# Kernel optimization log

Hardware: AMD Instinct MI355X
Metric: run time of the kernel (lower is better)

The kernel has to match this reference:

```python
import jax, jax.numpy as jnp
import numpy as np

DIM = 512
HEADS = 8
HEAD_DIM = DIM // HEADS
SCALE = HEAD_DIM ** -0.5
EPS = 1e-5


def _layernorm(x, w, b):
    mu = jnp.mean(x, axis=-1, keepdims=True)
    var = jnp.mean(jnp.square(x - mu), axis=-1, keepdims=True)
    return (x - mu) * jax.lax.rsqrt(var + EPS) * w + b


def setup_inputs() -> dict:
    key = jax.random.key(0)
    ks = jax.random.split(key, 9)
    B, Hs, Ws = 8, 32, 32
    r = jax.random.normal(ks[0], (B, DIM, Hs, Ws), dtype=jnp.float32)
    z = jax.random.normal(ks[1], (B, DIM, Hs, Ws), dtype=jnp.float32)
    w = lambda k: jax.random.normal(k, (DIM, DIM), dtype=jnp.float32) * 0.02
    return {
        "r": r,
        "z": z,
        "norm_r_w": jnp.ones((DIM,), jnp.float32),
        "norm_r_b": jnp.zeros((DIM,), jnp.float32),
        "norm_z_w": jnp.ones((DIM,), jnp.float32),
        "norm_z_b": jnp.zeros((DIM,), jnp.float32),
        "Wq": w(ks[2]),  # [out, in] torch Linear convention, no bias (qkv_bias=False)
        "Wk": w(ks[3]),
        "Wv": w(ks[4]),
        "Wa": w(ks[5]),
        "Wproj": w(ks[6]),
        "bproj": jax.random.normal(ks[7], (DIM,), dtype=jnp.float32) * 0.02,
    }


def reference(r, z, norm_r_w, norm_r_b, norm_z_w, norm_z_b, Wq, Wk, Wv, Wa, Wproj, bproj):
    z_sc = z
    B, C, Hz, Wz = z.shape
    # flatten(2).permute(0,2,1): NCHW -> [B, N, C]
    rf = r.reshape(B, C, -1).transpose(0, 2, 1)  # [B, Nr, C]
    zf = z.reshape(B, C, -1).transpose(0, 2, 1)  # [B, Nz, C]
    Nr, Nz = rf.shape[1], zf.shape[1]

    rf = _layernorm(rf, norm_r_w, norm_r_b)
    zf = _layernorm(zf, norm_z_w, norm_z_b)

    def heads(x, W, N):  # torch Linear: x @ W.T, then split heads -> [B,H,N,D]
        return (x @ W.T).reshape(B, N, HEADS, HEAD_DIM).transpose(0, 2, 1, 3)

    q = heads(rf, Wq, Nr)  # [B,H,Nr,D]
    k = heads(rf, Wk, Nr)  # [B,H,Nr,D]
    v = heads(zf, Wv, Nz)  # [B,H,Nz,D]
    a = heads(zf, Wa, Nz)  # [B,H,Nz,D]

    # stage 1: softmax(k @ a^T) @ v  -> anchor-aggregated values per r-token
    attn1 = jax.nn.softmax(jnp.einsum('bhnd,bhmd->bhnm', k, a) * SCALE, axis=-1)  # [B,H,Nr,Nz]
    v1 = jnp.einsum('bhnm,bhmd->bhnd', attn1, v)  # [B,H,Nr,D]

    # stage 2: softmax(a @ q^T) @ v1 -> outputs aligned with z tokens
    attn2 = jax.nn.softmax(jnp.einsum('bhmd,bhnd->bhmn', a, q) * SCALE, axis=-1)  # [B,H,Nz,Nr]
    out = jnp.einsum('bhmn,bhnd->bhmd', attn2, v1)  # [B,H,Nz,D]

    out = out.transpose(0, 2, 1, 3).reshape(B, Nz, C)
    out = out @ Wproj.T + bproj
    out = out.transpose(0, 2, 1).reshape(B, C, Hz, Wz)
    return out + z_sc
```

## Files before the change

### kernel.cpp

```cpp
#include <hip/hip_runtime.h>
#include <hip/hip_bf16.h>
#include <stdint.h>


using bf16 = __bf16;
typedef __bf16 bf16x4 __attribute__((ext_vector_type(4)));
typedef __bf16 bf16x8 __attribute__((ext_vector_type(8)));
typedef float f32x4 __attribute__((ext_vector_type(4)));
typedef float f32x16 __attribute__((ext_vector_type(16)));

#define DIMC 512
#define NTOK 1024
#define NB 8
#define NH 8
#define HD 64
#define SLABS 16

__device__ __forceinline__ void gload_lds16(const bf16* g, bf16* l) {
  __builtin_amdgcn_global_load_lds((__attribute__((address_space(1))) void*)g,
                                   (__attribute__((address_space(3))) void*)l,
                                   16, 0, 0);
}

__device__ __forceinline__ float bpermf(int srclane, float v) {
  int i = __builtin_amdgcn_ds_bpermute(srclane << 2, __builtin_bit_cast(int, v));
  return __builtin_bit_cast(float, i);
}

__device__ __forceinline__ int pkbf(float lo, float hi) {
  unsigned short a = __builtin_bit_cast(unsigned short, (bf16)lo);
  unsigned short b = __builtin_bit_cast(unsigned short, (bf16)hi);
  return (int)((unsigned)a | ((unsigned)b << 16));
}

__device__ __forceinline__ float fexp2(float x) {
  float r;
  asm("v_exp_f32 %0, %1" : "=v"(r) : "v"(x));
  return r;
}

__global__ __launch_bounds__(256) void k_ln_part(
    const float* __restrict__ r, const float* __restrict__ z, float* __restrict__ part) {
  int slab = blockIdx.x, b = blockIdx.y, tensor = blockIdx.z;
  const float* x = (tensor ? z : r) + ((size_t)b * DIMC + slab * 32) * NTOK + threadIdx.x * 4;
  float4 s = {0, 0, 0, 0}, ss = {0, 0, 0, 0};
#pragma unroll 8
  for (int c = 0; c < 32; ++c) {
    float4 v = *reinterpret_cast<const float4*>(x + (size_t)c * NTOK);
    s.x += v.x; s.y += v.y; s.z += v.z; s.w += v.w;
    ss.x += v.x * v.x; ss.y += v.y * v.y; ss.z += v.z * v.z; ss.w += v.w * v.w;
  }
  float* p = part + (((size_t)(tensor * 8 + b) * SLABS + slab) * 2) * NTOK + threadIdx.x * 4;
  *reinterpret_cast<float4*>(p) = s;
  *reinterpret_cast<float4*>(p + NTOK) = ss;
}

__global__ __launch_bounds__(256) void k_ln_fin(
    const float* __restrict__ part, float* __restrict__ mu, float* __restrict__ rs) {
  int t = blockIdx.x * 256 + threadIdx.x;
  int tb = t >> 10, n = t & 1023;
  const float* p = part + (size_t)tb * SLABS * 2 * NTOK + n;
  float s = 0.f, ss = 0.f;
#pragma unroll
  for (int i = 0; i < SLABS; ++i) {
    s += p[(size_t)i * 2 * NTOK];
    ss += p[(size_t)i * 2 * NTOK + NTOK];
  }
  float m = s * (1.0f / DIMC);
  mu[t] = m;
  rs[t] = rsqrtf(ss * (1.0f / DIMC) - m * m + 1e-5f);
}

__global__ __launch_bounds__(256) void k_ln_apply(
    const float* __restrict__ r, const float* __restrict__ z,
    const float* __restrict__ wr, const float* __restrict__ br,
    const float* __restrict__ wz, const float* __restrict__ bz,
    const float* __restrict__ mu, const float* __restrict__ rs,
    bf16* __restrict__ rf, bf16* __restrict__ zf) {
  __shared__ __align__(16) bf16 T[64 * 72];
  int bt = blockIdx.z;
  int tensor = bt & 1, b = bt >> 1;
  const float* x   = tensor ? z  : r;
  const float* w   = tensor ? wz : wr;
  const float* bia = tensor ? bz : br;
  bf16* out = tensor ? zf : rf;
  int n0 = blockIdx.x * 64, c0 = blockIdx.y * 64;
  const float* muP = mu + (tensor << 13) + (b << 10) + n0;
  const float* rsP = rs + (tensor << 13) + (b << 10) + n0;
  int tid = threadIdx.x;
  int cl = tid >> 3;
  int nl = (tid & 7) * 8;
#pragma unroll
  for (int pass = 0; pass < 2; ++pass) {
    int c = c0 + pass * 32 + cl;
    float wc = w[c], bc = bia[c];
    const float* src = x + ((size_t)(b * DIMC + c)) * NTOK + n0 + nl;
    float4 v0 = *reinterpret_cast<const float4*>(src);
    float4 v1 = *reinterpret_cast<const float4*>(src + 4);
    float vv[8] = {v0.x, v0.y, v0.z, v0.w, v1.x, v1.y, v1.z, v1.w};
#pragma unroll
    for (int j = 0; j < 8; ++j) {
      int n = nl + j;
      float val = (vv[j] - muP[n]) * rsP[n] * wc + bc;
      T[n * 72 + pass * 32 + cl] = (bf16)val;
    }
  }
  __syncthreads();
  int nr = tid >> 3;
  int cc = (tid & 7) * 8;
#pragma unroll
  for (int pass = 0; pass < 2; ++pass) {
    int n = pass * 32 + nr;
    bf16x8 o;
#pragma unroll
    for (int j = 0; j < 8; ++j) o[j] = T[n * 72 + cc + j];
    *reinterpret_cast<bf16x8*>(out + ((size_t)(b * NTOK + n0 + n)) * DIMC + c0 + cc) = o;
  }
}

__global__ __launch_bounds__(256) void k_cvt5(
    const float* __restrict__ W0, const float* __restrict__ W1,
    const float* __restrict__ W2, const float* __restrict__ W3,
    const float* __restrict__ W4, bf16* __restrict__ out) {
  int m = blockIdx.y;
  const float* W = (m == 0) ? W0 : (m == 1) ? W1 : (m == 2) ? W2 : (m == 3) ? W3 : W4;
  bf16* o = out + (size_t)m * DIMC * DIMC;
  int i = blockIdx.x * 256 + threadIdx.x;
  float4 v = reinterpret_cast<const float4*>(W)[i];
  bf16x4 b;
  b[0] = (bf16)v.x; b[1] = (bf16)v.y; b[2] = (bf16)v.z; b[3] = (bf16)v.w;
  *reinterpret_cast<bf16x4*>(o + (size_t)i * 4) = b;
}

template <int MODE>
__global__ __launch_bounds__(256) void k_gemm(
    const bf16* __restrict__ actA, const bf16* __restrict__ zf,
    const bf16* __restrict__ Wbf,
    void* __restrict__ outbase,
    const float* __restrict__ zres, const float* __restrict__ bproj) {
  __shared__ __align__(16) bf16 As[128 * 32];
  __shared__ __align__(16) bf16 Bs[128 * 32];
  int b = blockIdx.z;
  const bf16 *Ap, *Bp;
  int m0, n0;
  if (MODE == 0) {
    int mat = blockIdx.y;
    Ap = (mat < 2 ? actA : zf) + (size_t)b * NTOK * DIMC;
    int widx = (mat == 2) ? 3 : mat;
    Bp = Wbf + (size_t)widx * DIMC * DIMC;
    m0 = (blockIdx.x >> 2) * 128;
    n0 = (blockIdx.x & 3) * 128;
  } else {
    Ap = Wbf + (size_t)(MODE == 1 ? 4 : 2) * DIMC * DIMC;
    Bp = (MODE == 1 ? actA : zf) + (size_t)b * NTOK * DIMC;
    m0 = (blockIdx.x >> 3) * 128;
    n0 = (blockIdx.x & 7) * 128;
  }
  int tid = threadIdx.x;
  int w = tid >> 6, l = tid & 63;
  int wm = (w >> 1) * 64, wn = (w & 1) * 64;
  int lr = l & 15, lg = l >> 4;
  int srow = l >> 2;
  int scol = (l & 3) * 8;
  f32x4 acc[4][4] = {};

  for (int kt = 0; kt < 16; ++kt) {
    int k0 = kt * 32;
#pragma unroll
    for (int q = 0; q < 2; ++q) {
      int rowA = w * 32 + q * 16 + srow;
      gload_lds16(Ap + (size_t)(m0 + rowA) * DIMC + k0 + scol, &As[(w * 32 + q * 16) * 32]);
      gload_lds16(Bp + (size_t)(n0 + rowA) * DIMC + k0 + scol, &Bs[(w * 32 + q * 16) * 32]);
    }
    __syncthreads();
    bf16x8 af[4], bfr[4];
#pragma unroll
    for (int i = 0; i < 4; ++i)
      af[i] = *reinterpret_cast<const bf16x8*>(&As[(wm + 16 * i + lr) * 32 + lg * 8]);
#pragma unroll
    for (int j = 0; j < 4; ++j)
      bfr[j] = *reinterpret_cast<const bf16x8*>(&Bs[(wn + 16 * j + lr) * 32 + lg * 8]);
#pragma unroll
    for (int i = 0; i < 4; ++i)
#pragma unroll
      for (int j = 0; j < 4; ++j)
        acc[i][j] = __builtin_amdgcn_mfma_f32_16x16x32_bf16(af[i], bfr[j], acc[i][j], 0, 0, 0);
    __syncthreads();
  }

#pragma unroll
  for (int i = 0; i < 4; ++i) {
#pragma unroll
    for (int j = 0; j < 4; ++j) {
#pragma unroll
      for (int rr = 0; rr < 4; ++rr) {
        int mm = m0 + wm + 16 * i + lg * 4 + rr;
        int nn = n0 + wn + 16 * j + lr;
        if (MODE == 0) {
          bf16* outp = (bf16*)outbase + (size_t)blockIdx.y * ((size_t)NB * NH * NTOK * HD)
                       + (size_t)b * (NH * NTOK * HD);
          outp[((size_t)((nn >> 6) * NTOK + mm)) * HD + (nn & 63)] = (bf16)acc[i][j][rr];
        } else if (MODE == 2) {
          bf16* outp = (bf16*)outbase + (size_t)b * DIMC * NTOK;
          outp[(size_t)mm * NTOK + nn] = (bf16)acc[i][j][rr];
        } else {
          float* outp = (float*)outbase + (size_t)b * DIMC * NTOK;
          const float* zp = zres + (size_t)b * DIMC * NTOK;
          size_t idx = (size_t)mm * NTOK + nn;
          outp[idx] = acc[i][j][rr] + bproj[mm] + zp[idx];
        }
      }
    }
  }
}

__global__ __launch_bounds__(256) void k_flash6(
    const bf16* __restrict__ Qp, const bf16* __restrict__ Kp,
    const bf16* __restrict__ Vtp, bf16* __restrict__ Op, int out_mode) {
  __shared__ __align__(16) bf16 smem[16384];
  int tid = threadIdx.x;
  int w = tid >> 6, l = tid & 63;
  int hl = l >> 5, ln31 = l & 31;
  int id = blockIdx.x;
  int qt = (id >> 3) & 7;
  int bh = ((id & 7) << 3) | (id >> 6);
  int q0 = qt * 128;
  const bf16* Qb = Qp + (size_t)bh * NTOK * HD;
  const bf16* Kb = Kp + (size_t)bh * NTOK * HD;
  const bf16* Vb = Vtp + (size_t)bh * HD * NTOK;

  const float QS = 0.125f * 1.44269504088896340736f;
  bf16x8 qf[4];
  int qrow = q0 + w * 32 + ln31;
#pragma unroll
  for (int s = 0; s < 4; ++s) {
    bf16x8 raw = *reinterpret_cast<const bf16x8*>(Qb + (size_t)qrow * 64 + 16 * s + 8 * hl);
#pragma unroll
    for (int j = 0; j < 8; ++j) qf[s][j] = (bf16)((float)raw[j] * QS);
  }

  int koff0 = w * 16;
  int koff1 = w * 16 + 8;
  int fco = hl * 512 + ln31 * 8;

  {
    gload_lds16(Kb + (size_t)l * 64 + koff0, &smem[(2 * w) * 512]);
    gload_lds16(Kb + (size_t)l * 64 + koff1, &smem[(2 * w + 1) * 512]);
    gload_lds16(Vb + (size_t)l * 1024 + koff0, &smem[4096 + (2 * w) * 512]);
    gload_lds16(Vb + (size_t)l * 1024 + koff1, &smem[4096 + (2 * w + 1) * 512]);
  }

  float l_run = 0.f;
  f32x16 of0{}, of1{};

#pragma unroll 1
  for (int kt = 0; kt < 16; ++kt) {
    __syncthreads();
    int buf = (kt & 1) ? 8192 : 0;

    if (kt + 1 < 16) {
      int k0n = (kt + 1) * 64;
      int nb = buf ^ 8192;
      gload_lds16(Kb + (size_t)(k0n + l) * 64 + koff0, &smem[nb + (2 * w) * 512]);
      gload_lds16(Kb + (size_t)(k0n + l) * 64 + koff1, &smem[nb + (2 * w + 1) * 512]);
      gload_lds16(Vb + (size_t)l * 1024 + k0n + koff0, &smem[nb + 4096 + (2 * w) * 512]);
      gload_lds16(Vb + (size_t)l * 1024 + k0n + koff1, &smem[nb + 4096 + (2 * w + 1) * 512]);
    }

    const bf16* Ks = &smem[buf];
    const bf16* Vs = &smem[buf + 4096];

    bf16x8 kf0[4], kf1[4];
#pragma unroll
    for (int s = 0; s < 4; ++s) {
      kf0[s] = *reinterpret_cast<const bf16x8*>(&Ks[s * 1024 + fco]);
      kf1[s] = *reinterpret_cast<const bf16x8*>(&Ks[s * 1024 + fco + 256]);
    }

    f32x16 sT0, sT1;
#pragma unroll
    for (int r = 0; r < 16; ++r) { sT0[r] = -16.0f; sT1[r] = -16.0f; }
    __builtin_amdgcn_s_setprio(1);
#pragma unroll
    for (int s = 0; s < 4; ++s) {
      sT0 = __builtin_amdgcn_mfma_f32_32x32x16_bf16(kf0[s], qf[s], sT0, 0, 0, 0);
      sT1 = __builtin_amdgcn_mfma_f32_32x32x16_bf16(kf1[s], qf[s], sT1, 0, 0, 0);
    }
    __builtin_amdgcn_s_setprio(0);

    float s0 = 0.f, s1 = 0.f, s2 = 0.f, s3 = 0.f;
#pragma unroll
    for (int r = 0; r < 16; r += 4) {
      sT0[r]     = fexp2(sT0[r]);     s0 += sT0[r];
      sT0[r + 1] = fexp2(sT0[r + 1]); s1 += sT0[r + 1];
      sT0[r + 2] = fexp2(sT0[r + 2]); s2 += sT0[r + 2];
      sT0[r + 3] = fexp2(sT0[r + 3]); s3 += sT0[r + 3];
      sT1[r]     = fexp2(sT1[r]);     s0 += sT1[r];
      sT1[r + 1] = fexp2(sT1[r + 1]); s1 += sT1[r + 1];
      sT1[r + 2] = fexp2(sT1[r + 2]); s2 += sT1[r + 2];
      sT1[r + 3] = fexp2(sT1[r + 3]); s3 += sT1[r + 3];
    }
    float lsum = (s0 + s1) + (s2 + s3);
    lsum += __shfl_xor(lsum, 32);
    l_run += lsum;

    bf16x8 vf0[4], vf1[4];
#pragma unroll
    for (int ks = 0; ks < 4; ++ks) {
      vf0[ks] = *reinterpret_cast<const bf16x8*>(&Vs[ks * 1024 + fco]);
      vf1[ks] = *reinterpret_cast<const bf16x8*>(&Vs[ks * 1024 + fco + 256]);
    }

    int wpk[16];
#pragma unroll
    for (int g = 0; g < 4; ++g) {
      wpk[2 * g]     = pkbf(sT0[4 * g],     sT0[4 * g + 1]);
      wpk[2 * g + 1] = pkbf(sT0[4 * g + 2], sT0[4 * g + 3]);
      wpk[2 * (g + 4)]     = pkbf(sT1[4 * g],     sT1[4 * g + 1]);
      wpk[2 * (g + 4) + 1] = pkbf(sT1[4 * g + 2], sT1[4 * g + 3]);
    }
    int rw[16];
#pragma unroll
    for (int t = 0; t < 16; ++t) rw[t] = __shfl_xor(wpk[t], 32);

    bf16x8 pf[4];
#pragma unroll
    for (int ks = 0; ks < 4; ++ks) {
      int gA = 2 * ks, gB = 2 * ks + 1;
      union { int i[4]; bf16x8 v; } u;
      u.i[0] = hl ? rw[2 * gB]     : wpk[2 * gA];
      u.i[1] = hl ? rw[2 * gB + 1] : wpk[2 * gA + 1];
      u.i[2] = hl ? wpk[2 * gB]     : rw[2 * gA];
      u.i[3] = hl ? wpk[2 * gB + 1] : rw[2 * gA + 1];
      pf[ks] = u.v;
    }

    __builtin_amdgcn_s_setprio(1);
#pragma unroll
    for (int ks = 0; ks < 4; ++ks) {
      of0 = __builtin_amdgcn_mfma_f32_32x32x16_bf16(pf[ks], vf0[ks], of0, 0, 0, 0);
      of1 = __builtin_amdgcn_mfma_f32_32x32x16_bf16(pf[ks], vf1[ks], of1, 0, 0, 0);
    }
    __builtin_amdgcn_s_setprio(0);
  }

  __syncthreads();
  float inv = 1.0f / l_run;
  if (out_mode == 0) {
    bf16* T = &smem[w * 2560];
#pragma unroll
    for (int r = 0; r < 16; ++r) {
      int qloc = (r & 3) + 8 * (r >> 2) + 4 * hl;
      float invr = bpermf(qloc + (l & 32), inv);
      T[ln31 * 40 + qloc] = (bf16)(of0[r] * invr);
      T[(ln31 + 32) * 40 + qloc] = (bf16)(of1[r] * invr);
    }
#pragma unroll
    for (int i = 0; i < 4; ++i) {
      int d = (l >> 2) + 16 * i;
      int qc = (l & 3) * 8;
      bf16x8 v = *reinterpret_cast<const bf16x8*>(&T[d * 40 + qc]);
      *reinterpret_cast<bf16x8*>(Op + ((size_t)bh * HD + d) * NTOK + q0 + w * 32 + qc) = v;
    }
  } else {
#pragma unroll
    for (int r = 0; r < 16; ++r) {
      int qloc = (r & 3) + 8 * (r >> 2) + 4 * hl;
      float invr = bpermf(qloc + (l & 32), inv);
      int q = q0 + w * 32 + qloc;
      int b = bh >> 3, h = bh & 7;
      bf16* p = Op + ((size_t)(b * NTOK + q)) * DIMC + h * 64;
      p[ln31] = (bf16)(of0[r] * invr);
      p[ln31 + 32] = (bf16)(of1[r] * invr);
    }
  }
}

extern "C" void kernel_launch(void* const* d_in, const int* in_sizes, int n_in,
                              void* d_out, int out_size, void* d_ws, size_t ws_size,
                              hipStream_t stream) {
  const float* r  = (const float*)d_in[0];
  const float* z  = (const float*)d_in[1];
  const float* wr = (const float*)d_in[2];
  const float* br = (const float*)d_in[3];
  const float* wz = (const float*)d_in[4];
  const float* bz = (const float*)d_in[5];
  const float* Wq = (const float*)d_in[6];
  const float* Wk = (const float*)d_in[7];
  const float* Wv = (const float*)d_in[8];
  const float* Wa = (const float*)d_in[9];
  const float* Wp = (const float*)d_in[10];
  const float* bp = (const float*)d_in[11];

  char* ws = (char*)d_ws;
  float* mu = (float*)ws;
  float* rs = (float*)(ws + 65536);
  bf16* rf   = (bf16*)(ws + 131072);
  bf16* zf   = rf + (size_t)NB * NTOK * DIMC;
  bf16* qka  = zf + (size_t)NB * NTOK * DIMC;
  const size_t SLOT = (size_t)NB * NH * NTOK * HD;
  bf16* vt  = qka + 3 * SLOT;
  bf16* v1t = qka + 4 * SLOT;
  bf16* at2 = v1t + SLOT;
  bf16* Wbf = at2 + SLOT;

  bf16* Qt = qka;
  bf16* Kt = qka + 1 * SLOT;
  bf16* At = qka + 2 * SLOT;

  float* part = (float*)at2;

  k_ln_part<<<dim3(SLABS, NB, 2), 256, 0, stream>>>(r, z, part);
  k_ln_fin<<<64, 256, 0, stream>>>(part, mu, rs);
  k_ln_apply<<<dim3(16, 8, 16), 256, 0, stream>>>(r, z, wr, br, wz, bz, mu, rs, rf, zf);
  k_cvt5<<<dim3(256, 5), 256, 0, stream>>>(Wq, Wk, Wv, Wa, Wp, Wbf);
  k_gemm<0><<<dim3(32, 3, NB), 256, 0, stream>>>(rf, zf, Wbf, qka, nullptr, nullptr);
  k_gemm<2><<<dim3(32, 1, NB), 256, 0, stream>>>(nullptr, zf, Wbf, vt, nullptr, nullptr);
  k_flash6<<<512, 256, 0, stream>>>(Kt, At, vt, v1t, 0);
  k_flash6<<<512, 256, 0, stream>>>(At, Qt, v1t, at2, 1);
  k_gemm<1><<<dim3(32, 1, NB), 256, 0, stream>>>(at2, nullptr, Wbf, d_out, z, bp);
}
```

Measured before the change: 139.6 us.

## Fuse layernorm kernels, merge V-projection GEMM, shrink flash tiles to 64 queries

Three LayerNorm kernels are replaced by one kernel per 64-token block that computes the statistics and applies the normalisation, removing the partial-sum round trip through global memory and two launches. The V projection GEMM is folded into the QKA GEMM launch as a fourth grid slice. The flash attention kernel now uses 128-thread blocks with 64 queries each, doubling the block count, and defers the cross-half row-sum shuffle to the end of the loop. Risks: the fused LN reads each input twice with strided per-channel loads and serialises eight channel chunks per block, and the smaller flash blocks reload K/V tiles more often.

```diff
diff --git a/kernel.cpp b/kernel.cpp
--- a/kernel.cpp
+++ b/kernel.cpp
@@ -14,7 +14,6 @@
 #define NB 8
 #define NH 8
 #define HD 64
-#define SLABS 16
 
 __device__ __forceinline__ void gload_lds16(const bf16* g, bf16* l) {
   __builtin_amdgcn_global_load_lds((__attribute__((address_space(1))) void*)g,
@@ -39,82 +38,71 @@
   return r;
 }
 
-__global__ __launch_bounds__(256) void k_ln_part(
-    const float* __restrict__ r, const float* __restrict__ z, float* __restrict__ part) {
-  int slab = blockIdx.x, b = blockIdx.y, tensor = blockIdx.z;
-  const float* x = (tensor ? z : r) + ((size_t)b * DIMC + slab * 32) * NTOK + threadIdx.x * 4;
-  float4 s = {0, 0, 0, 0}, ss = {0, 0, 0, 0};
-#pragma unroll 8
-  for (int c = 0; c < 32; ++c) {
-    float4 v = *reinterpret_cast<const float4*>(x + (size_t)c * NTOK);
-    s.x += v.x; s.y += v.y; s.z += v.z; s.w += v.w;
-    ss.x += v.x * v.x; ss.y += v.y * v.y; ss.z += v.z * v.z; ss.w += v.w * v.w;
-  }
-  float* p = part + (((size_t)(tensor * 8 + b) * SLABS + slab) * 2) * NTOK + threadIdx.x * 4;
-  *reinterpret_cast<float4*>(p) = s;
-  *reinterpret_cast<float4*>(p + NTOK) = ss;
-}
-
-__global__ __launch_bounds__(256) void k_ln_fin(
-    const float* __restrict__ part, float* __restrict__ mu, float* __restrict__ rs) {
-  int t = blockIdx.x * 256 + threadIdx.x;
-  int tb = t >> 10, n = t & 1023;
-  const float* p = part + (size_t)tb * SLABS * 2 * NTOK + n;
-  float s = 0.f, ss = 0.f;
-#pragma unroll
-  for (int i = 0; i < SLABS; ++i) {
-    s += p[(size_t)i * 2 * NTOK];
-    ss += p[(size_t)i * 2 * NTOK + NTOK];
-  }
-  float m = s * (1.0f / DIMC);
-  mu[t] = m;
-  rs[t] = rsqrtf(ss * (1.0f / DIMC) - m * m + 1e-5f);
-}
-
-__global__ __launch_bounds__(256) void k_ln_apply(
+__global__ __launch_bounds__(256) void k_ln_fused(
     const float* __restrict__ r, const float* __restrict__ z,
     const float* __restrict__ wr, const float* __restrict__ br,
     const float* __restrict__ wz, const float* __restrict__ bz,
-    const float* __restrict__ mu, const float* __restrict__ rs,
     bf16* __restrict__ rf, bf16* __restrict__ zf) {
+  __shared__ float sp[4][64], ssq[4][64];
+  __shared__ float muS[64], rsS[64];
   __shared__ __align__(16) bf16 T[64 * 72];
-  int bt = blockIdx.z;
-  int tensor = bt & 1, b = bt >> 1;
+  int n0 = blockIdx.x * 64, b = blockIdx.y, tensor = blockIdx.z;
   const float* x   = tensor ? z  : r;
   const float* w   = tensor ? wz : wr;
   const float* bia = tensor ? bz : br;
   bf16* out = tensor ? zf : rf;
-  int n0 = blockIdx.x * 64, c0 = blockIdx.y * 64;
-  const float* muP = mu + (tensor << 13) + (b << 10) + n0;
-  const float* rsP = rs + (tensor << 13) + (b << 10) + n0;
   int tid = threadIdx.x;
+
+  {
+    int n = tid & 63, grp = tid >> 6;
+    const float* xp = x + ((size_t)(b * DIMC + grp * 128)) * NTOK + n0 + n;
+    float s = 0.f, ss = 0.f;
+#pragma unroll 8
+    for (int c = 0; c < 128; ++c) {
+      float v = xp[(size_t)c * NTOK];
+      s += v; ss += v * v;
+    }
+    sp[grp][n] = s; ssq[grp][n] = ss;
+  }
+  __syncthreads();
+  if (tid < 64) {
+    float s  = sp[0][tid] + sp[1][tid] + sp[2][tid] + sp[3][tid];
+    float ss = ssq[0][tid] + ssq[1][tid] + ssq[2][tid] + ssq[3][tid];
+    float m = s * (1.0f / DIMC);
+    muS[tid] = m;
+    rsS[tid] = rsqrtf(ss * (1.0f / DIMC) - m * m + 1e-5f);
+  }
+  __syncthreads();
+
   int cl = tid >> 3;
   int nl = (tid & 7) * 8;
-#pragma unroll
-  for (int pass = 0; pass < 2; ++pass) {
-    int c = c0 + pass * 32 + cl;
-    float wc = w[c], bc = bia[c];
-    const float* src = x + ((size_t)(b * DIMC + c)) * NTOK + n0 + nl;
-    float4 v0 = *reinterpret_cast<const float4*>(src);
-    float4 v1 = *reinterpret_cast<const float4*>(src + 4);
-    float vv[8] = {v0.x, v0.y, v0.z, v0.w, v1.x, v1.y, v1.z, v1.w};
-#pragma unroll
-    for (int j = 0; j < 8; ++j) {
-      int n = nl + j;
-      float val = (vv[j] - muP[n]) * rsP[n] * wc + bc;
-      T[n * 72 + pass * 32 + cl] = (bf16)val;
-    }
-  }
-  __syncthreads();
-  int nr = tid >> 3;
-  int cc = (tid & 7) * 8;
-#pragma unroll
-  for (int pass = 0; pass < 2; ++pass) {
-    int n = pass * 32 + nr;
-    bf16x8 o;
-#pragma unroll
-    for (int j = 0; j < 8; ++j) o[j] = T[n * 72 + cc + j];
-    *reinterpret_cast<bf16x8*>(out + ((size_t)(b * NTOK + n0 + n)) * DIMC + c0 + cc) = o;
+  for (int cs = 0; cs < 8; ++cs) {
+    int c0 = cs * 64;
+#pragma unroll
+    for (int pass = 0; pass < 2; ++pass) {
+      int c = c0 + pass * 32 + cl;
+      float wc = w[c], bc = bia[c];
+      const float* src = x + ((size_t)(b * DIMC + c)) * NTOK + n0 + nl;
+      float4 v0 = *reinterpret_cast<const float4*>(src);
+      float4 v1 = *reinterpret_cast<const float4*>(src + 4);
+      float vv[8] = {v0.x, v0.y, v0.z, v0.w, v1.x, v1.y, v1.z, v1.w};
+#pragma unroll
+      for (int j = 0; j < 8; ++j) {
+        int n = nl + j;
+        float val = (vv[j] - muS[n]) * rsS[n] * wc + bc;
+        T[n * 72 + pass * 32 + cl] = (bf16)val;
+      }
+    }
+    __syncthreads();
+#pragma unroll
+    for (int pass = 0; pass < 2; ++pass) {
+      int n = pass * 32 + cl;
+      bf16x8 o;
+#pragma unroll
+      for (int j = 0; j < 8; ++j) o[j] = T[n * 72 + nl + j];
+      *reinterpret_cast<bf16x8*>(out + ((size_t)(b * NTOK + n0 + n)) * DIMC + c0 + nl) = o;
+    }
+    __syncthreads();
   }
 }
 
@@ -143,8 +131,8 @@
   int b = blockIdx.z;
   const bf16 *Ap, *Bp;
   int m0, n0;
-  if (MODE == 0) {
-    int mat = blockIdx.y;
+  int mat = (MODE == 0) ? blockIdx.y : -1;
+  if (MODE == 0 && mat < 3) {
     Ap = (mat < 2 ? actA : zf) + (size_t)b * NTOK * DIMC;
     int widx = (mat == 2) ? 3 : mat;
     Bp = Wbf + (size_t)widx * DIMC * DIMC;
@@ -188,6 +176,7 @@
     __syncthreads();
   }
 
+  const size_t SLOT = (size_t)NB * NH * NTOK * HD;
 #pragma unroll
   for (int i = 0; i < 4; ++i) {
 #pragma unroll
@@ -196,12 +185,11 @@
       for (int rr = 0; rr < 4; ++rr) {
         int mm = m0 + wm + 16 * i + lg * 4 + rr;
         int nn = n0 + wn + 16 * j + lr;
-        if (MODE == 0) {
-          bf16* outp = (bf16*)outbase + (size_t)blockIdx.y * ((size_t)NB * NH * NTOK * HD)
-                       + (size_t)b * (NH * NTOK * HD);
+        if (MODE == 0 && mat < 3) {
+          bf16* outp = (bf16*)outbase + (size_t)mat * SLOT + (size_t)b * (NH * NTOK * HD);
           outp[((size_t)((nn >> 6) * NTOK + mm)) * HD + (nn & 63)] = (bf16)acc[i][j][rr];
-        } else if (MODE == 2) {
-          bf16* outp = (bf16*)outbase + (size_t)b * DIMC * NTOK;
+        } else if (MODE == 0) {
+          bf16* outp = (bf16*)outbase + 3 * SLOT + (size_t)b * DIMC * NTOK;
           outp[(size_t)mm * NTOK + nn] = (bf16)acc[i][j][rr];
         } else {
           float* outp = (float*)outbase + (size_t)b * DIMC * NTOK;
@@ -214,7 +202,7 @@
   }
 }
 
-__global__ __launch_bounds__(256) void k_flash6(
+__global__ __launch_bounds__(128) void k_flash7(
     const bf16* __restrict__ Qp, const bf16* __restrict__ Kp,
     const bf16* __restrict__ Vtp, bf16* __restrict__ Op, int out_mode) {
   __shared__ __align__(16) bf16 smem[16384];
@@ -222,9 +210,9 @@
   int w = tid >> 6, l = tid & 63;
   int hl = l >> 5, ln31 = l & 31;
   int id = blockIdx.x;
-  int qt = (id >> 3) & 7;
-  int bh = ((id & 7) << 3) | (id >> 6);
-  int q0 = qt * 128;
+  int qt = (id >> 3) & 15;
+  int bh = ((id & 7) << 3) | (id >> 7);
+  int q0 = qt * 64;
   const bf16* Qb = Qp + (size_t)bh * NTOK * HD;
   const bf16* Kb = Kp + (size_t)bh * NTOK * HD;
   const bf16* Vb = Vtp + (size_t)bh * HD * NTOK;
@@ -239,15 +227,14 @@
     for (int j = 0; j < 8; ++j) qf[s][j] = (bf16)((float)raw[j] * QS);
   }
 
-  int koff0 = w * 16;
-  int koff1 = w * 16 + 8;
   int fco = hl * 512 + ln31 * 8;
 
-  {
-    gload_lds16(Kb + (size_t)l * 64 + koff0, &smem[(2 * w) * 512]);
-    gload_lds16(Kb + (size_t)l * 64 + koff1, &smem[(2 * w + 1) * 512]);
-    gload_lds16(Vb + (size_t)l * 1024 + koff0, &smem[4096 + (2 * w) * 512]);
-    gload_lds16(Vb + (size_t)l * 1024 + koff1, &smem[4096 + (2 * w + 1) * 512]);
+#pragma unroll
+  for (int gg = 0; gg < 4; ++gg) {
+    int g = 4 * w + gg;
+    int koff = (g >> 1) * 16 + (g & 1) * 8;
+    gload_lds16(Kb + (size_t)l * 64 + koff, &smem[g * 512]);
+    gload_lds16(Vb + (size_t)l * 1024 + koff, &smem[4096 + g * 512]);
   }
 
   float l_run = 0.f;
@@ -261,10 +248,13 @@
     if (kt + 1 < 16) {
       int k0n = (kt + 1) * 64;
       int nb = buf ^ 8192;
-      gload_lds16(Kb + (size_t)(k0n + l) * 64 + koff0, &smem[nb + (2 * w) * 512]);
-      gload_lds16(Kb + (size_t)(k0n + l) * 64 + koff1, &smem[nb + (2 * w + 1) * 512]);
-      gload_lds16(Vb + (size_t)l * 1024 + k0n + koff0, &smem[nb + 4096 + (2 * w) * 512]);
-      gload_lds16(Vb + (size_t)l * 1024 + k0n + koff1, &smem[nb + 4096 + (2 * w + 1) * 512]);
+#pragma unroll
+      for (int gg = 0; gg < 4; ++gg) {
+        int g = 4 * w + gg;
+        int koff = (g >> 1) * 16 + (g & 1) * 8;
+        gload_lds16(Kb + (size_t)(k0n + l) * 64 + koff, &smem[nb + g * 512]);
+        gload_lds16(Vb + (size_t)l * 1024 + k0n + koff, &smem[nb + 4096 + g * 512]);
+      }
     }
 
     const bf16* Ks = &smem[buf];
@@ -300,9 +290,7 @@
       sT1[r + 2] = fexp2(sT1[r + 2]); s2 += sT1[r + 2];
       sT1[r + 3] = fexp2(sT1[r + 3]); s3 += sT1[r + 3];
     }
-    float lsum = (s0 + s1) + (s2 + s3);
-    lsum += __shfl_xor(lsum, 32);
-    l_run += lsum;
+    l_run += (s0 + s1) + (s2 + s3);
 
     bf16x8 vf0[4], vf1[4];
 #pragma unroll
@@ -345,7 +333,8 @@
   }
 
   __syncthreads();
-  float inv = 1.0f / l_run;
+  float lt = l_run + __shfl_xor(l_run, 32);
+  float inv = 1.0f / lt;
   if (out_mode == 0) {
     bf16* T = &smem[w * 2560];
 #pragma unroll
@@ -393,9 +382,7 @@
   const float* bp = (const float*)d_in[11];
 
   char* ws = (char*)d_ws;
-  float* mu = (float*)ws;
-  float* rs = (float*)(ws + 65536);
-  bf16* rf   = (bf16*)(ws + 131072);
+  bf16* rf   = (bf16*)ws;
   bf16* zf   = rf + (size_t)NB * NTOK * DIMC;
   bf16* qka  = zf + (size_t)NB * NTOK * DIMC;
   const size_t SLOT = (size_t)NB * NH * NTOK * HD;
@@ -408,15 +395,10 @@
   bf16* Kt = qka + 1 * SLOT;
   bf16* At = qka + 2 * SLOT;
 
-  float* part = (float*)at2;
-
-  k_ln_part<<<dim3(SLABS, NB, 2), 256, 0, stream>>>(r, z, part);
-  k_ln_fin<<<64, 256, 0, stream>>>(part, mu, rs);
-  k_ln_apply<<<dim3(16, 8, 16), 256, 0, stream>>>(r, z, wr, br, wz, bz, mu, rs, rf, zf);
+  k_ln_fused<<<dim3(16, NB, 2), 256, 0, stream>>>(r, z, wr, br, wz, bz, rf, zf);
   k_cvt5<<<dim3(256, 5), 256, 0, stream>>>(Wq, Wk, Wv, Wa, Wp, Wbf);
-  k_gemm<0><<<dim3(32, 3, NB), 256, 0, stream>>>(rf, zf, Wbf, qka, nullptr, nullptr);
-  k_gemm<2><<<dim3(32, 1, NB), 256, 0, stream>>>(nullptr, zf, Wbf, vt, nullptr, nullptr);
-  k_flash6<<<512, 256, 0, stream>>>(Kt, At, vt, v1t, 0);
-  k_flash6<<<512, 256, 0, stream>>>(At, Qt, v1t, at2, 1);
+  k_gemm<0><<<dim3(32, 4, NB), 256, 0, stream>>>(rf, zf, Wbf, qka, nullptr, nullptr);
+  k_flash7<<<1024, 128, 0, stream>>>(Kt, At, vt, v1t, 0);
+  k_flash7<<<1024, 128, 0, stream>>>(At, Qt, v1t, at2, 1);
   k_gemm<1><<<dim3(32, 1, NB), 256, 0, stream>>>(at2, nullptr, Wbf, d_out, z, bp);
 }
```

After: 152.3 us. 9.1% more time.
